# Kernel optimization log

Measured on AMD Instinct MI355X. Metric: run time of the kernel, lower is better.

The kernel has to match this reference:

```python
import jax, jax.numpy as jnp
import numpy as np

FEATURES = 4
HIDDEN = 32


def setup_inputs() -> dict:
    key = jax.random.key(0)
    ks = jax.random.split(key, 12)
    n_nodes, n_edges = 100000, 2500000
    x = jax.random.normal(ks[0], (n_nodes, FEATURES), dtype=jnp.float32)
    edge_index = jax.random.randint(ks[1], (2, n_edges), 0, n_nodes, dtype=jnp.int64)
    def glorot(k, fan_in, fan_out):
        s = jnp.sqrt(6.0 / (fan_in + fan_out)).astype(jnp.float32)
        return jax.random.uniform(k, (fan_in, fan_out), jnp.float32, -s, s)
    return {
        "x": x,
        "edge_index": edge_index,
        "W1": glorot(ks[2], FEATURES, HIDDEN), "b1": jnp.zeros((HIDDEN,), jnp.float32),
        "W2": glorot(ks[3], HIDDEN, HIDDEN),   "b2": jnp.zeros((HIDDEN,), jnp.float32),
        "W21": glorot(ks[4], HIDDEN, HIDDEN),  "b21": jnp.zeros((HIDDEN,), jnp.float32),
        "W3": glorot(ks[5], HIDDEN, 1),        "b3": jnp.zeros((1,), jnp.float32),
    }


def _gcn_norm(edge_index, n_nodes):
    # Add self-loops, compute symmetric normalization deg^-1/2[dst]*deg^-1/2[src]
    loops = jnp.arange(n_nodes, dtype=edge_index.dtype)
    src = jnp.concatenate([edge_index[0], loops])
    dst = jnp.concatenate([edge_index[1], loops])
    deg = jax.ops.segment_sum(jnp.ones_like(dst, dtype=jnp.float32), dst, num_segments=n_nodes)
    dinv = jnp.where(deg > 0, jax.lax.rsqrt(deg), 0.0)
    norm = dinv[src] * dinv[dst]  # [E+N]
    return src, dst, norm


def _gcn_layer(x, W, b, src, dst, norm, n_nodes):
    h = x @ W                                   # [N, out]
    msg = h[src] * norm[:, None]                # gather + scale
    out = jax.ops.segment_sum(msg, dst, num_segments=n_nodes)  # scatter-add
    return out + b


def reference(x, edge_index, W1, b1, W2, b2, W21, b21, W3, b3):
    n_nodes = x.shape[0]
    src, dst, norm = _gcn_norm(edge_index, n_nodes)
    h = jax.nn.relu(_gcn_layer(x, W1, b1, src, dst, norm, n_nodes))
    h = jax.nn.relu(_gcn_layer(h, W2, b2, src, dst, norm, n_nodes))
    h = jax.nn.relu(_gcn_layer(h, W21, b21, src, dst, norm, n_nodes))
    return _gcn_layer(h, W3, b3, src, dst, norm, n_nodes)
```

## Files before the change

kernel.cpp:

```cpp
#include <hip/hip_runtime.h>

#define FEATS 4
#define HID 32
#define BLK 256
#define CAP 64
#define PW 256
#define PSHIFT 8
#define PCAP 8192
#define NPB 512
#define PBLK 1024
#define MAXK 8
#define MAXNP 512

static inline int cdiv(long long a, int b) { return (int)((a + b - 1) / b); }

__global__ void k_zero_i(int* __restrict__ p, int n) {
    int i = blockIdx.x * blockDim.x + threadIdx.x;
    if (i < n) p[i] = 0;
}

__global__ void __launch_bounds__(PBLK, 4)
k_partition(const int* __restrict__ src, const int* __restrict__ dst,
            int* __restrict__ part_fill, unsigned int* __restrict__ part_edges,
            int e, int np) {
    __shared__ int lcnt[MAXNP];
    __shared__ int lbase[MAXNP];
    for (int p = threadIdx.x; p < np; p += blockDim.x) lcnt[p] = 0;
    __syncthreads();
    int chunk = (e + gridDim.x - 1) / gridDim.x;
    int lo = blockIdx.x * chunk;
    int hi = min(lo + chunk, e);
    unsigned pw[MAXK];
    int pp[MAXK];
#pragma unroll
    for (int k = 0; k < MAXK; k++) {
        int j = lo + threadIdx.x + k * (int)blockDim.x;
        if (j < hi) {
            int d = dst[j], s = src[j];
            int p = d >> PSHIFT;
            pp[k] = p;
            pw[k] = (unsigned)s | ((unsigned)(d & (PW - 1)) << 24);
            atomicAdd(&lcnt[p], 1);
        } else pp[k] = -1;
    }
    __syncthreads();
    for (int p = threadIdx.x; p < np; p += blockDim.x) {
        int c = lcnt[p];
        lbase[p] = c ? atomicAdd(&part_fill[p], c) : 0;
        lcnt[p] = 0;
    }
    __syncthreads();
#pragma unroll
    for (int k = 0; k < MAXK; k++) {
        if (pp[k] >= 0) {
            int p = pp[k];
            int pos = lbase[p] + atomicAdd(&lcnt[p], 1);
            if (pos < PCAP) part_edges[(size_t)p * PCAP + pos] = pw[k];
        }
    }
}

__global__ void k_local_csr(const int* __restrict__ part_fill,
                            const unsigned int* __restrict__ part_edges,
                            int* __restrict__ cnt_g, float* __restrict__ dinv,
                            int* __restrict__ bucket, int n) {
    __shared__ int cnt[PW];
    int p = blockIdx.x;
    if (threadIdx.x < PW) cnt[threadIdx.x] = 0;
    __syncthreads();
    int m = min(part_fill[p], PCAP);
    const unsigned int* pe = part_edges + (size_t)p * PCAP;
    int base_node = p << PSHIFT;
    for (int j = threadIdx.x; j < m; j += blockDim.x) {
        unsigned v = pe[j];
        int local = (int)(v >> 24);
        int s = (int)(v & 0xFFFFFFu);
        int pos = atomicAdd(&cnt[local], 1);
        if (pos < CAP) bucket[(size_t)(base_node + local) * CAP + pos] = s;
    }
    __syncthreads();
    if (threadIdx.x < PW) {
        int node = base_node + threadIdx.x;
        if (node < n) {
            int dg = cnt[threadIdx.x];
            cnt_g[node] = dg;
            dinv[node] = rsqrtf((float)(dg + 1));
        }
    }
}

__global__ void k_dinv(const int* __restrict__ deg, float* __restrict__ dinv, int n) {
    int i = blockIdx.x * blockDim.x + threadIdx.x;
    if (i < n) dinv[i] = rsqrtf((float)(deg[i] + 1));
}

__global__ void k_xn0(const float4* __restrict__ x, const float* __restrict__ dinv,
                      float4* __restrict__ xn, int n) {
    int i = blockIdx.x * blockDim.x + threadIdx.x;
    if (i < n) {
        float4 v = x[i];
        float s = dinv[i];
        v.x *= s; v.y *= s; v.z *= s; v.w *= s;
        xn[i] = v;
    }
}

__global__ void k_gather4(const int* __restrict__ cnt, const int* __restrict__ bucket,
                          const float4* __restrict__ xn, const float* __restrict__ dinv,
                          float4* __restrict__ agg, int n) {
    int gid = blockIdx.x * blockDim.x + threadIdx.x;
    int node = gid >> 3;
    int lane = gid & 7;
    if (node >= n) return;
    int dg = min(cnt[node], CAP);
    const int* row = bucket + (size_t)node * CAP;
    float4 acc = make_float4(0.f, 0.f, 0.f, 0.f);
    int j = lane;
    for (; j + 8 < dg; j += 16) {
        int s0 = row[j], s1 = row[j + 8];
        float4 v0 = xn[s0];
        float4 v1 = xn[s1];
        acc.x += v0.x + v1.x; acc.y += v0.y + v1.y;
        acc.z += v0.z + v1.z; acc.w += v0.w + v1.w;
    }
    if (j < dg) {
        float4 v = xn[row[j]];
        acc.x += v.x; acc.y += v.y; acc.z += v.z; acc.w += v.w;
    }
#pragma unroll
    for (int o = 4; o > 0; o >>= 1) {
        acc.x += __shfl_down(acc.x, o, 8);
        acc.y += __shfl_down(acc.y, o, 8);
        acc.z += __shfl_down(acc.z, o, 8);
        acc.w += __shfl_down(acc.w, o, 8);
    }
    if (lane == 0) {
        float4 self = xn[node];
        float sc = dinv[node];
        float4 r;
        r.x = sc * (acc.x + self.x);
        r.y = sc * (acc.y + self.y);
        r.z = sc * (acc.z + self.z);
        r.w = sc * (acc.w + self.w);
        agg[node] = r;
    }
}

__global__ void k_fuse12(const float4* __restrict__ agg4,
                         const float* __restrict__ W1, const float* __restrict__ b1,
                         const float* __restrict__ W2, const float* __restrict__ dinv,
                         float* __restrict__ hn, int n) {
    __shared__ float4 sW1[FEATS * 8];
    __shared__ float4 sB1[8];
    __shared__ float4 sW2[HID * 8];
    int tid = threadIdx.x;
    if (tid < FEATS * 8) sW1[tid] = ((const float4*)W1)[tid];
    if (tid < 8) sB1[tid] = ((const float4*)b1)[tid];
    for (int i = tid; i < HID * 8; i += blockDim.x) sW2[i] = ((const float4*)W2)[i];
    __syncthreads();
    int node = blockIdx.x * blockDim.x + tid;
    if (node >= n) return;
    float4 a = agg4[node];
    float4 y4[8];
#pragma unroll
    for (int k4 = 0; k4 < 8; k4++) {
        float4 r = sB1[k4];
        float4 w0 = sW1[0 * 8 + k4], w1 = sW1[1 * 8 + k4];
        float4 w2 = sW1[2 * 8 + k4], w3 = sW1[3 * 8 + k4];
        r.x += a.x * w0.x + a.y * w1.x + a.z * w2.x + a.w * w3.x;
        r.y += a.x * w0.y + a.y * w1.y + a.z * w2.y + a.w * w3.y;
        r.z += a.x * w0.z + a.y * w1.z + a.z * w2.z + a.w * w3.z;
        r.w += a.x * w0.w + a.y * w1.w + a.z * w2.w + a.w * w3.w;
        r.x = fmaxf(r.x, 0.f); r.y = fmaxf(r.y, 0.f);
        r.z = fmaxf(r.z, 0.f); r.w = fmaxf(r.w, 0.f);
        y4[k4] = r;
    }
    float4 acc[8];
#pragma unroll
    for (int c4 = 0; c4 < 8; c4++) acc[c4] = make_float4(0.f, 0.f, 0.f, 0.f);
#pragma unroll
    for (int k4 = 0; k4 < 8; k4++) {
        float4 yv = y4[k4];
#pragma unroll
        for (int c4 = 0; c4 < 8; c4++) {
            float4 wa = sW2[(4 * k4 + 0) * 8 + c4];
            float4 wb = sW2[(4 * k4 + 1) * 8 + c4];
            float4 wc = sW2[(4 * k4 + 2) * 8 + c4];
            float4 wd = sW2[(4 * k4 + 3) * 8 + c4];
            acc[c4].x += yv.x * wa.x + yv.y * wb.x + yv.z * wc.x + yv.w * wd.x;
            acc[c4].y += yv.x * wa.y + yv.y * wb.y + yv.z * wc.y + yv.w * wd.y;
            acc[c4].z += yv.x * wa.z + yv.y * wb.z + yv.z * wc.z + yv.w * wd.z;
            acc[c4].w += yv.x * wa.w + yv.y * wb.w + yv.z * wc.w + yv.w * wd.w;
        }
    }
    float sc = dinv[node];
    float4* op = (float4*)hn + (size_t)node * 8;
#pragma unroll
    for (int c4 = 0; c4 < 8; c4++) {
        float4 r = acc[c4];
        r.x *= sc; r.y *= sc; r.z *= sc; r.w *= sc;
        op[c4] = r;
    }
}

template <int K, int C>
__global__ void k_mm(const float* __restrict__ in, const float* __restrict__ W,
                     const float* __restrict__ dinv, float* __restrict__ hn, int n) {
    __shared__ float sW[K * C];
    for (int i = threadIdx.x; i < K * C; i += blockDim.x) sW[i] = W[i];
    __syncthreads();
    int gid = blockIdx.x * blockDim.x + threadIdx.x;
    int node = gid / C, c = gid % C;
    if (node >= n) return;
    float acc = 0.0f;
#pragma unroll
    for (int k = 0; k < K; k++) acc += in[node * K + k] * sW[k * C + c];
    hn[node * C + c] = acc * dinv[node];
}

#define ACC4(v) do { acc.x += (v).x; acc.y += (v).y; acc.z += (v).z; acc.w += (v).w; } while (0)

#define GATHER_BODY()                                                        \
    int dg = min(cnt[node], CAP);                                            \
    const float4* hp = (const float4*)hn;                                    \
    const int* row = bucket + (size_t)node * CAP;                            \
    float4 acc = hp[node * 8 + cq];                                          \
    int j = 0;                                                               \
    for (; j + 8 <= dg; j += 8) {                                            \
        int4 sa = *(const int4*)(row + j);                                   \
        int4 sb = *(const int4*)(row + j + 4);                               \
        float4 v0 = hp[sa.x * 8 + cq];                                       \
        float4 v1 = hp[sa.y * 8 + cq];                                       \
        float4 v2 = hp[sa.z * 8 + cq];                                       \
        float4 v3 = hp[sa.w * 8 + cq];                                       \
        float4 v4 = hp[sb.x * 8 + cq];                                       \
        float4 v5 = hp[sb.y * 8 + cq];                                       \
        float4 v6 = hp[sb.z * 8 + cq];                                       \
        float4 v7 = hp[sb.w * 8 + cq];                                       \
        ACC4(v0); ACC4(v1); ACC4(v2); ACC4(v3);                              \
        ACC4(v4); ACC4(v5); ACC4(v6); ACC4(v7);                              \
    }                                                                        \
    if (j + 4 <= dg) {                                                       \
        int4 s4 = *(const int4*)(row + j);                                   \
        float4 v0 = hp[s4.x * 8 + cq];                                       \
        float4 v1 = hp[s4.y * 8 + cq];                                       \
        float4 v2 = hp[s4.z * 8 + cq];                                       \
        float4 v3 = hp[s4.w * 8 + cq];                                       \
        ACC4(v0); ACC4(v1); ACC4(v2); ACC4(v3);                              \
        j += 4;                                                              \
    }                                                                        \
    for (; j < dg; j++) {                                                    \
        float4 v = hp[row[j] * 8 + cq];                                      \
        ACC4(v);                                                             \
    }

__global__ void k_gather_fmm(const int* __restrict__ cnt, const int* __restrict__ bucket,
                             const float* __restrict__ hn, const float* __restrict__ dinv,
                             const float* __restrict__ bias, const float* __restrict__ Wn,
                             float* __restrict__ hn3, int n) {
    __shared__ float4 sW[HID * 8];
    sW[threadIdx.x] = ((const float4*)Wn)[threadIdx.x];
    __syncthreads();
    int gid = blockIdx.x * blockDim.x + threadIdx.x;
    int node = gid >> 3;
    int cq = gid & 7;
    if (node >= n) return;
    GATHER_BODY()
    float sc = dinv[node];
    float4 b = ((const float4*)bias)[cq];
    float4 y;
    y.x = fmaxf(sc * acc.x + b.x, 0.f);
    y.y = fmaxf(sc * acc.y + b.y, 0.f);
    y.z = fmaxf(sc * acc.z + b.z, 0.f);
    y.w = fmaxf(sc * acc.w + b.w, 0.f);
    float4 o = make_float4(0.f, 0.f, 0.f, 0.f);
#pragma unroll
    for (int r = 0; r < 8; r++) {
        float4 v;
        v.x = __shfl(y.x, r, 8);
        v.y = __shfl(y.y, r, 8);
        v.z = __shfl(y.z, r, 8);
        v.w = __shfl(y.w, r, 8);
        float4 w0 = sW[(4 * r + 0) * 8 + cq];
        float4 w1 = sW[(4 * r + 1) * 8 + cq];
        float4 w2 = sW[(4 * r + 2) * 8 + cq];
        float4 w3 = sW[(4 * r + 3) * 8 + cq];
        o.x += v.x * w0.x + v.y * w1.x + v.z * w2.x + v.w * w3.x;
        o.y += v.x * w0.y + v.y * w1.y + v.z * w2.y + v.w * w3.y;
        o.z += v.x * w0.z + v.y * w1.z + v.z * w2.z + v.w * w3.z;
        o.w += v.x * w0.w + v.y * w1.w + v.z * w2.w + v.w * w3.w;
    }
    o.x *= sc; o.y *= sc; o.z *= sc; o.w *= sc;
    ((float4*)hn3)[node * 8 + cq] = o;
}

__global__ void k_gather_fdot(const int* __restrict__ cnt, const int* __restrict__ bucket,
                              const float* __restrict__ hn, const float* __restrict__ dinv,
                              const float* __restrict__ bias, const float* __restrict__ W3,
                              float* __restrict__ hn4, int n) {
    int gid = blockIdx.x * blockDim.x + threadIdx.x;
    int node = gid >> 3;
    int cq = gid & 7;
    if (node >= n) return;
    GATHER_BODY()
    float sc = dinv[node];
    float4 b = ((const float4*)bias)[cq];
    float4 w = ((const float4*)W3)[cq];
    float p = fmaxf(sc * acc.x + b.x, 0.f) * w.x
            + fmaxf(sc * acc.y + b.y, 0.f) * w.y
            + fmaxf(sc * acc.z + b.z, 0.f) * w.z
            + fmaxf(sc * acc.w + b.w, 0.f) * w.w;
#pragma unroll
    for (int o = 4; o > 0; o >>= 1) p += __shfl_down(p, o, 8);
    if (cq == 0) hn4[node] = p * sc;
}

__global__ void k_gather1b(const int* __restrict__ cnt, const int* __restrict__ bucket,
                           const float* __restrict__ hn, const float* __restrict__ dinv,
                           const float* __restrict__ b, float* __restrict__ out, int n) {
    int gid = blockIdx.x * blockDim.x + threadIdx.x;
    int node = gid >> 3;
    int lane = gid & 7;
    if (node >= n) return;
    int dg = min(cnt[node], CAP);
    const int* row = bucket + (size_t)node * CAP;
    float acc = (lane == 0) ? hn[node] : 0.0f;
    int j = lane;
    for (; j + 8 < dg; j += 16) {
        float a0 = hn[row[j]];
        float a1 = hn[row[j + 8]];
        acc += a0 + a1;
    }
    if (j < dg) acc += hn[row[j]];
#pragma unroll
    for (int o = 4; o > 0; o >>= 1) acc += __shfl_down(acc, o, 8);
    if (lane == 0) out[node] = dinv[node] * acc + b[0];
}

__global__ void k_deg_count(const int* __restrict__ dst, int* __restrict__ deg, int e) {
    int i = blockIdx.x * blockDim.x + threadIdx.x;
    if (i < e) atomicAdd(&deg[dst[i]], 1);
}

__global__ void k_block_scan(const int* __restrict__ deg, int* __restrict__ exc,
                             int* __restrict__ blk_sums, int n) {
    __shared__ int s[BLK];
    int i = blockIdx.x * BLK + threadIdx.x;
    int v = (i < n) ? deg[i] : 0;
    s[threadIdx.x] = v;
    __syncthreads();
    for (int off = 1; off < BLK; off <<= 1) {
        int t = (threadIdx.x >= (unsigned)off) ? s[threadIdx.x - off] : 0;
        __syncthreads();
        s[threadIdx.x] += t;
        __syncthreads();
    }
    if (i < n) exc[i] = s[threadIdx.x] - v;
    if (threadIdx.x == BLK - 1) blk_sums[blockIdx.x] = s[threadIdx.x];
}

__global__ void k_scan_sums(int* __restrict__ blk_sums, int nb) {
    __shared__ int s[1024];
    __shared__ int carry;
    if (threadIdx.x == 0) carry = 0;
    __syncthreads();
    for (int base = 0; base < nb; base += 1024) {
        int i = base + threadIdx.x;
        int v = (i < nb) ? blk_sums[i] : 0;
        s[threadIdx.x] = v;
        __syncthreads();
        for (int off = 1; off < 1024; off <<= 1) {
            int t = (threadIdx.x >= (unsigned)off) ? s[threadIdx.x - off] : 0;
            __syncthreads();
            s[threadIdx.x] += t;
            __syncthreads();
        }
        if (i < nb) blk_sums[i] = s[threadIdx.x] - v + carry;
        __syncthreads();
        if (threadIdx.x == 0) carry += s[1023];
        __syncthreads();
    }
}

__global__ void k_add_off(const int* __restrict__ exc, const int* __restrict__ blk_sums,
                          int* __restrict__ row_start, int* __restrict__ fill, int n) {
    int i = blockIdx.x * blockDim.x + threadIdx.x;
    if (i < n) {
        int rs = exc[i] + blk_sums[i / BLK];
        row_start[i] = rs;
        fill[i] = rs;
    }
}

__global__ void k_scatter(const int* __restrict__ src, const int* __restrict__ dst,
                          int* __restrict__ fill, int* __restrict__ csr_src, int e) {
    int i = blockIdx.x * blockDim.x + threadIdx.x;
    if (i < e) {
        int pos = atomicAdd(&fill[dst[i]], 1);
        csr_src[pos] = src[i];
    }
}

template <bool RELU>
__global__ void k_gather32(const int* __restrict__ row_start, const int* __restrict__ deg,
                           const int* __restrict__ csr_src, const float* __restrict__ hn,
                           const float* __restrict__ dinv, const float* __restrict__ bias,
                           float* __restrict__ y, int n) {
    int gid = blockIdx.x * blockDim.x + threadIdx.x;
    int node = gid >> 3;
    int cq = gid & 7;
    if (node >= n) return;
    int rs = row_start[node], dg = deg[node];
    const float4* hp = (const float4*)hn;
    float4 acc = hp[node * 8 + cq];
    for (int j = 0; j < dg; j++) {
        int s = csr_src[rs + j];
        float4 v = hp[s * 8 + cq];
        ACC4(v);
    }
    float sc = dinv[node];
    float4 b = ((const float4*)bias)[cq];
    float4 r;
    r.x = sc * acc.x + b.x; r.y = sc * acc.y + b.y;
    r.z = sc * acc.z + b.z; r.w = sc * acc.w + b.w;
    if (RELU) {
        r.x = fmaxf(r.x, 0.0f); r.y = fmaxf(r.y, 0.0f);
        r.z = fmaxf(r.z, 0.0f); r.w = fmaxf(r.w, 0.0f);
    }
    ((float4*)y)[node * 8 + cq] = r;
}

__global__ void k_gather1(const int* __restrict__ row_start, const int* __restrict__ deg,
                          const int* __restrict__ csr_src, const float* __restrict__ hn,
                          const float* __restrict__ dinv, const float* __restrict__ b,
                          float* __restrict__ out, int n) {
    int gid = blockIdx.x * blockDim.x + threadIdx.x;
    int node = gid >> 3;
    int lane = gid & 7;
    if (node >= n) return;
    int rs = row_start[node], dg = deg[node];
    float acc = (lane == 0) ? hn[node] : 0.0f;
    for (int j = lane; j < dg; j += 8) acc += hn[csr_src[rs + j]];
#pragma unroll
    for (int o = 4; o > 0; o >>= 1) acc += __shfl_down(acc, o, 8);
    if (lane == 0) out[node] = dinv[node] * acc + b[0];
}

extern "C" void kernel_launch(void* const* d_in, const int* in_sizes, int n_in,
                              void* d_out, int out_size, void* d_ws, size_t ws_size,
                              hipStream_t stream) {
    const float* x   = (const float*)d_in[0];
    const int*   ei  = (const int*)d_in[1];
    const float* W1  = (const float*)d_in[2];
    const float* b1  = (const float*)d_in[3];
    const float* W2  = (const float*)d_in[4];
    const float* b2  = (const float*)d_in[5];
    const float* W21 = (const float*)d_in[6];
    const float* b21 = (const float*)d_in[7];
    const float* W3  = (const float*)d_in[8];
    const float* b3  = (const float*)d_in[9];
    float* out = (float*)d_out;

    const int n = in_sizes[0] / FEATS;
    const int e = in_sizes[1] / 2;
    const int* src = ei;
    const int* dst = ei + e;
    const int nb = cdiv(n, BLK);
    const int np = cdiv(n, PW);

    auto align256 = [](size_t v) { return (v + 255) & ~(size_t)255; };
    const long long n8 = (long long)n * 8;

    size_t sz_cnt    = align256((size_t)n * 4);
    size_t sz_dinv   = align256((size_t)n * 4);
    size_t sz_f4     = align256((size_t)n * 16);
    size_t sz_bucket = align256((size_t)n * CAP * 4);
    size_t sz_hn     = align256((size_t)n * HID * 4);
    size_t sz_part   = align256((size_t)np * PCAP * 4) + align256((size_t)np * 4);
    size_t region    = 2 * sz_hn > sz_part ? 2 * sz_hn : sz_part;
    size_t need = sz_cnt + sz_dinv + 2 * sz_f4 + sz_bucket + region;

    if (ws_size >= need && np <= MAXNP && (long long)e <= (long long)NPB * PBLK * MAXK) {
        char* ws = (char*)d_ws;
        size_t off = 0;
        int*    cnt_g  = (int*)(ws + off);    off += sz_cnt;
        float*  dinv   = (float*)(ws + off);  off += sz_dinv;
        float4* xn     = (float4*)(ws + off); off += sz_f4;
        float4* agg4   = (float4*)(ws + off); off += sz_f4;
        int*    bucket = (int*)(ws + off);    off += sz_bucket;
        char*   reg    = ws + off;
        float* hn = (float*)reg;
        float* yb = (float*)(reg + sz_hn);
        unsigned int* part_edges = (unsigned int*)reg;
        int* part_fill = (int*)(reg + align256((size_t)np * PCAP * 4));

        k_zero_i<<<cdiv(np, BLK), BLK, 0, stream>>>(part_fill, np);
        k_partition<<<NPB, PBLK, 0, stream>>>(src, dst, part_fill, part_edges, e, np);
        k_local_csr<<<np, PBLK, 0, stream>>>(part_fill, part_edges, cnt_g, dinv, bucket, n);

        k_xn0<<<nb, BLK, 0, stream>>>((const float4*)x, dinv, xn, n);
        k_gather4<<<cdiv(n8, BLK), BLK, 0, stream>>>(cnt_g, bucket, xn, dinv, agg4, n);
        k_fuse12<<<nb, BLK, 0, stream>>>(agg4, W1, b1, W2, dinv, hn, n);

        k_gather_fmm<<<cdiv(n8, BLK), BLK, 0, stream>>>(cnt_g, bucket, hn, dinv, b2, W21, yb, n);
        k_gather_fdot<<<cdiv(n8, BLK), BLK, 0, stream>>>(cnt_g, bucket, yb, dinv, b21, W3, hn, n);
        k_gather1b<<<cdiv(n8, BLK), BLK, 0, stream>>>(cnt_g, bucket, hn, dinv, b3, out, n);
    } else {
        const long long nc = (long long)n * HID;
        char* ws = (char*)d_ws;
        size_t off = 0;
        int*   deg_i     = (int*)(ws + off);   off += align256((size_t)n * 4);
        int*   exc       = (int*)(ws + off);   off += align256((size_t)n * 4);
        int*   row_start = (int*)(ws + off);   off += align256((size_t)n * 4);
        int*   fill      = (int*)(ws + off);   off += align256((size_t)n * 4);
        int*   blk_sums  = (int*)(ws + off);   off += align256((size_t)nb * 4);
        float* dinv      = (float*)(ws + off); off += align256((size_t)n * 4);
        int*   csr_src   = (int*)(ws + off);   off += align256((size_t)e * 4);
        float* hn        = (float*)(ws + off); off += align256((size_t)n * HID * 4);
        float* yb        = (float*)(ws + off); off += align256((size_t)n * HID * 4);

        k_zero_i<<<nb, BLK, 0, stream>>>(deg_i, n);
        k_deg_count<<<cdiv(e, BLK), BLK, 0, stream>>>(dst, deg_i, e);
        k_dinv<<<nb, BLK, 0, stream>>>(deg_i, dinv, n);
        k_block_scan<<<nb, BLK, 0, stream>>>(deg_i, exc, blk_sums, n);
        k_scan_sums<<<1, 1024, 0, stream>>>(blk_sums, nb);
        k_add_off<<<nb, BLK, 0, stream>>>(exc, blk_sums, row_start, fill, n);
        k_scatter<<<cdiv(e, BLK), BLK, 0, stream>>>(src, dst, fill, csr_src, e);

        k_mm<FEATS, HID><<<cdiv(nc, BLK), BLK, 0, stream>>>(x, W1, dinv, hn, n);
        k_gather32<true><<<cdiv(n8, BLK), BLK, 0, stream>>>(row_start, deg_i, csr_src, hn, dinv, b1, yb, n);

        k_mm<HID, HID><<<cdiv(nc, BLK), BLK, 0, stream>>>(yb, W2, dinv, hn, n);
        k_gather32<true><<<cdiv(n8, BLK), BLK, 0, stream>>>(row_start, deg_i, csr_src, hn, dinv, b2, yb, n);

        k_mm<HID, HID><<<cdiv(nc, BLK), BLK, 0, stream>>>(yb, W21, dinv, hn, n);
        k_gather32<true><<<cdiv(n8, BLK), BLK, 0, stream>>>(row_start, deg_i, csr_src, hn, dinv, b21, yb, n);

        k_mm<HID, 1><<<cdiv(n, BLK), BLK, 0, stream>>>(yb, W3, dinv, hn, n);
        k_gather1<<<cdiv(n8, BLK), BLK, 0, stream>>>(row_start, deg_i, csr_src, hn, dinv, b3, out, n);
    }
}
```

Before: 252.6 us.

## Fuse x prescale into local CSR and layer-1 gather with dense layers

Folds the x*dinv prescale into the local CSR build kernel, so the separate k_xn0 launch goes away. Merges the layer-1 neighbor gather with the W1/ReLU/W2 transform: the 8 lanes per node all-reduce with xor shuffles, each lane computes one quarter-column group of the hidden vector, and they exchange values by shuffle for the 32x32 matmul. This removes two kernel launches and the agg4 round trip through memory. It also spreads the per-node dense work across 8 lanes instead of one thread, at the cost of extra shuffles.

```diff
diff --git a/kernel.cpp b/kernel.cpp
--- a/kernel.cpp
+++ b/kernel.cpp
@@ -62,8 +62,9 @@
 
 __global__ void k_local_csr(const int* __restrict__ part_fill,
                             const unsigned int* __restrict__ part_edges,
+                            const float4* __restrict__ x,
                             int* __restrict__ cnt_g, float* __restrict__ dinv,
-                            int* __restrict__ bucket, int n) {
+                            float4* __restrict__ xn, int* __restrict__ bucket, int n) {
     __shared__ int cnt[PW];
     int p = blockIdx.x;
     if (threadIdx.x < PW) cnt[threadIdx.x] = 0;
@@ -84,7 +85,11 @@
         if (node < n) {
             int dg = cnt[threadIdx.x];
             cnt_g[node] = dg;
-            dinv[node] = rsqrtf((float)(dg + 1));
+            float s = rsqrtf((float)(dg + 1));
+            dinv[node] = s;
+            float4 v = x[node];
+            v.x *= s; v.y *= s; v.z *= s; v.w *= s;
+            xn[node] = v;
         }
     }
 }
@@ -94,28 +99,26 @@
     if (i < n) dinv[i] = rsqrtf((float)(deg[i] + 1));
 }
 
-__global__ void k_xn0(const float4* __restrict__ x, const float* __restrict__ dinv,
-                      float4* __restrict__ xn, int n) {
-    int i = blockIdx.x * blockDim.x + threadIdx.x;
-    if (i < n) {
-        float4 v = x[i];
-        float s = dinv[i];
-        v.x *= s; v.y *= s; v.z *= s; v.w *= s;
-        xn[i] = v;
-    }
-}
-
-__global__ void k_gather4(const int* __restrict__ cnt, const int* __restrict__ bucket,
-                          const float4* __restrict__ xn, const float* __restrict__ dinv,
-                          float4* __restrict__ agg, int n) {
-    int gid = blockIdx.x * blockDim.x + threadIdx.x;
+__global__ void k_gather4_f12(const int* __restrict__ cnt, const int* __restrict__ bucket,
+                              const float4* __restrict__ xn, const float* __restrict__ dinv,
+                              const float* __restrict__ W1, const float* __restrict__ b1,
+                              const float* __restrict__ W2, float* __restrict__ hn, int n) {
+    __shared__ float4 sW1[FEATS * 8];
+    __shared__ float4 sB1[8];
+    __shared__ float4 sW2[HID * 8];
+    int tid = threadIdx.x;
+    if (tid < FEATS * 8) sW1[tid] = ((const float4*)W1)[tid];
+    if (tid < 8) sB1[tid] = ((const float4*)b1)[tid];
+    sW2[tid] = ((const float4*)W2)[tid];
+    __syncthreads();
+    int gid = blockIdx.x * blockDim.x + tid;
     int node = gid >> 3;
-    int lane = gid & 7;
+    int cq = gid & 7;
     if (node >= n) return;
     int dg = min(cnt[node], CAP);
     const int* row = bucket + (size_t)node * CAP;
     float4 acc = make_float4(0.f, 0.f, 0.f, 0.f);
-    int j = lane;
+    int j = cq;
     for (; j + 8 < dg; j += 16) {
         int s0 = row[j], s1 = row[j + 8];
         float4 v0 = xn[s0];
@@ -128,79 +131,47 @@
         acc.x += v.x; acc.y += v.y; acc.z += v.z; acc.w += v.w;
     }
 #pragma unroll
-    for (int o = 4; o > 0; o >>= 1) {
-        acc.x += __shfl_down(acc.x, o, 8);
-        acc.y += __shfl_down(acc.y, o, 8);
-        acc.z += __shfl_down(acc.z, o, 8);
-        acc.w += __shfl_down(acc.w, o, 8);
-    }
-    if (lane == 0) {
-        float4 self = xn[node];
-        float sc = dinv[node];
-        float4 r;
-        r.x = sc * (acc.x + self.x);
-        r.y = sc * (acc.y + self.y);
-        r.z = sc * (acc.z + self.z);
-        r.w = sc * (acc.w + self.w);
-        agg[node] = r;
-    }
-}
-
-__global__ void k_fuse12(const float4* __restrict__ agg4,
-                         const float* __restrict__ W1, const float* __restrict__ b1,
-                         const float* __restrict__ W2, const float* __restrict__ dinv,
-                         float* __restrict__ hn, int n) {
-    __shared__ float4 sW1[FEATS * 8];
-    __shared__ float4 sB1[8];
-    __shared__ float4 sW2[HID * 8];
-    int tid = threadIdx.x;
-    if (tid < FEATS * 8) sW1[tid] = ((const float4*)W1)[tid];
-    if (tid < 8) sB1[tid] = ((const float4*)b1)[tid];
-    for (int i = tid; i < HID * 8; i += blockDim.x) sW2[i] = ((const float4*)W2)[i];
-    __syncthreads();
-    int node = blockIdx.x * blockDim.x + tid;
-    if (node >= n) return;
-    float4 a = agg4[node];
-    float4 y4[8];
-#pragma unroll
-    for (int k4 = 0; k4 < 8; k4++) {
-        float4 r = sB1[k4];
-        float4 w0 = sW1[0 * 8 + k4], w1 = sW1[1 * 8 + k4];
-        float4 w2 = sW1[2 * 8 + k4], w3 = sW1[3 * 8 + k4];
-        r.x += a.x * w0.x + a.y * w1.x + a.z * w2.x + a.w * w3.x;
-        r.y += a.x * w0.y + a.y * w1.y + a.z * w2.y + a.w * w3.y;
-        r.z += a.x * w0.z + a.y * w1.z + a.z * w2.z + a.w * w3.z;
-        r.w += a.x * w0.w + a.y * w1.w + a.z * w2.w + a.w * w3.w;
-        r.x = fmaxf(r.x, 0.f); r.y = fmaxf(r.y, 0.f);
-        r.z = fmaxf(r.z, 0.f); r.w = fmaxf(r.w, 0.f);
-        y4[k4] = r;
-    }
-    float4 acc[8];
-#pragma unroll
-    for (int c4 = 0; c4 < 8; c4++) acc[c4] = make_float4(0.f, 0.f, 0.f, 0.f);
-#pragma unroll
-    for (int k4 = 0; k4 < 8; k4++) {
-        float4 yv = y4[k4];
-#pragma unroll
-        for (int c4 = 0; c4 < 8; c4++) {
-            float4 wa = sW2[(4 * k4 + 0) * 8 + c4];
-            float4 wb = sW2[(4 * k4 + 1) * 8 + c4];
-            float4 wc = sW2[(4 * k4 + 2) * 8 + c4];
-            float4 wd = sW2[(4 * k4 + 3) * 8 + c4];
-            acc[c4].x += yv.x * wa.x + yv.y * wb.x + yv.z * wc.x + yv.w * wd.x;
-            acc[c4].y += yv.x * wa.y + yv.y * wb.y + yv.z * wc.y + yv.w * wd.y;
-            acc[c4].z += yv.x * wa.z + yv.y * wb.z + yv.z * wc.z + yv.w * wd.z;
-            acc[c4].w += yv.x * wa.w + yv.y * wb.w + yv.z * wc.w + yv.w * wd.w;
-        }
+    for (int m = 1; m < 8; m <<= 1) {
+        acc.x += __shfl_xor(acc.x, m, 8);
+        acc.y += __shfl_xor(acc.y, m, 8);
+        acc.z += __shfl_xor(acc.z, m, 8);
+        acc.w += __shfl_xor(acc.w, m, 8);
     }
     float sc = dinv[node];
-    float4* op = (float4*)hn + (size_t)node * 8;
-#pragma unroll
-    for (int c4 = 0; c4 < 8; c4++) {
-        float4 r = acc[c4];
-        r.x *= sc; r.y *= sc; r.z *= sc; r.w *= sc;
-        op[c4] = r;
-    }
+    float4 self = xn[node];
+    float4 a;
+    a.x = sc * (acc.x + self.x);
+    a.y = sc * (acc.y + self.y);
+    a.z = sc * (acc.z + self.z);
+    a.w = sc * (acc.w + self.w);
+    float4 w0 = sW1[0 * 8 + cq], w1 = sW1[1 * 8 + cq];
+    float4 w2 = sW1[2 * 8 + cq], w3 = sW1[3 * 8 + cq];
+    float4 y = sB1[cq];
+    y.x += a.x * w0.x + a.y * w1.x + a.z * w2.x + a.w * w3.x;
+    y.y += a.x * w0.y + a.y * w1.y + a.z * w2.y + a.w * w3.y;
+    y.z += a.x * w0.z + a.y * w1.z + a.z * w2.z + a.w * w3.z;
+    y.w += a.x * w0.w + a.y * w1.w + a.z * w2.w + a.w * w3.w;
+    y.x = fmaxf(y.x, 0.f); y.y = fmaxf(y.y, 0.f);
+    y.z = fmaxf(y.z, 0.f); y.w = fmaxf(y.w, 0.f);
+    float4 o = make_float4(0.f, 0.f, 0.f, 0.f);
+#pragma unroll
+    for (int r = 0; r < 8; r++) {
+        float4 v;
+        v.x = __shfl(y.x, r, 8);
+        v.y = __shfl(y.y, r, 8);
+        v.z = __shfl(y.z, r, 8);
+        v.w = __shfl(y.w, r, 8);
+        float4 wa = sW2[(4 * r + 0) * 8 + cq];
+        float4 wb = sW2[(4 * r + 1) * 8 + cq];
+        float4 wc = sW2[(4 * r + 2) * 8 + cq];
+        float4 wd = sW2[(4 * r + 3) * 8 + cq];
+        o.x += v.x * wa.x + v.y * wb.x + v.z * wc.x + v.w * wd.x;
+        o.y += v.x * wa.y + v.y * wb.y + v.z * wc.y + v.w * wd.y;
+        o.z += v.x * wa.z + v.y * wb.z + v.z * wc.z + v.w * wd.z;
+        o.w += v.x * wa.w + v.y * wb.w + v.z * wc.w + v.w * wd.w;
+    }
+    o.x *= sc; o.y *= sc; o.z *= sc; o.w *= sc;
+    ((float4*)hn)[node * 8 + cq] = o;
 }
 
 template <int K, int C>
@@ -478,7 +449,7 @@
     size_t sz_hn     = align256((size_t)n * HID * 4);
     size_t sz_part   = align256((size_t)np * PCAP * 4) + align256((size_t)np * 4);
     size_t region    = 2 * sz_hn > sz_part ? 2 * sz_hn : sz_part;
-    size_t need = sz_cnt + sz_dinv + 2 * sz_f4 + sz_bucket + region;
+    size_t need = sz_cnt + sz_dinv + sz_f4 + sz_bucket + region;
 
     if (ws_size >= need && np <= MAXNP && (long long)e <= (long long)NPB * PBLK * MAXK) {
         char* ws = (char*)d_ws;
@@ -486,7 +457,6 @@
         int*    cnt_g  = (int*)(ws + off);    off += sz_cnt;
         float*  dinv   = (float*)(ws + off);  off += sz_dinv;
         float4* xn     = (float4*)(ws + off); off += sz_f4;
-        float4* agg4   = (float4*)(ws + off); off += sz_f4;
         int*    bucket = (int*)(ws + off);    off += sz_bucket;
         char*   reg    = ws + off;
         float* hn = (float*)reg;
@@ -496,11 +466,11 @@
 
         k_zero_i<<<cdiv(np, BLK), BLK, 0, stream>>>(part_fill, np);
         k_partition<<<NPB, PBLK, 0, stream>>>(src, dst, part_fill, part_edges, e, np);
-        k_local_csr<<<np, PBLK, 0, stream>>>(part_fill, part_edges, cnt_g, dinv, bucket, n);
-
-        k_xn0<<<nb, BLK, 0, stream>>>((const float4*)x, dinv, xn, n);
-        k_gather4<<<cdiv(n8, BLK), BLK, 0, stream>>>(cnt_g, bucket, xn, dinv, agg4, n);
-        k_fuse12<<<nb, BLK, 0, stream>>>(agg4, W1, b1, W2, dinv, hn, n);
+        k_local_csr<<<np, PBLK, 0, stream>>>(part_fill, part_edges, (const float4*)x,
+                                             cnt_g, dinv, xn, bucket, n);
+
+        k_gather4_f12<<<cdiv(n8, BLK), BLK, 0, stream>>>(cnt_g, bucket, xn, dinv,
+                                                         W1, b1, W2, hn, n);
 
         k_gather_fmm<<<cdiv(n8, BLK), BLK, 0, stream>>>(cnt_g, bucket, hn, dinv, b2, W21, yb, n);
         k_gather_fdot<<<cdiv(n8, BLK), BLK, 0, stream>>>(cnt_g, bucket, yb, dinv, b21, W3, hn, n);
```

New measurement: 243.7 us, median of 2. -3.5%, faster.
